# Optimization experiments

Hardware: AMD Instinct MI355X
Metric: run time of the kernel (lower is better)

## Reference

```python
import jax, jax.numpy as jnp
import numpy as np

BN_EPS = 1e-5


def setup_inputs() -> dict:
    key = jax.random.key(0)
    ks = jax.random.split(key, 6)
    N, E, D_IN, D_OUT = 100000, 625000, 128, 128
    x = jax.random.normal(ks[0], (N, D_IN), dtype=jnp.float32)
    edge_index = jax.random.randint(ks[1], (2, E), 0, N, dtype=jnp.int64)
    # Glorot-style init for GCNConv weight, uniform for linear (values only matter for correctness testing)
    W = jax.random.normal(ks[2], (D_IN, D_OUT), dtype=jnp.float32) * (1.0 / np.sqrt(D_IN))
    b = jnp.zeros((D_OUT,), dtype=jnp.float32)
    res_W = jax.random.normal(ks[3], (D_IN, D_OUT), dtype=jnp.float32) * (1.0 / np.sqrt(D_IN))
    res_b = jnp.zeros((D_OUT,), dtype=jnp.float32)
    bn_gamma = jnp.ones((D_OUT,), dtype=jnp.float32)
    bn_beta = jnp.zeros((D_OUT,), dtype=jnp.float32)
    return {"x": x, "edge_index": edge_index, "W": W, "b": b,
            "res_W": res_W, "res_b": res_b, "bn_gamma": bn_gamma, "bn_beta": bn_beta}


def _gcn_forward(x, edge_index, W, b, res_W, res_b, bn_gamma, bn_beta):
    N = x.shape[0]
    # ---- GCNConv: add self-loops, symmetric degree normalization (PyG defaults) ----
    loops = jnp.arange(N, dtype=edge_index.dtype)
    src = jnp.concatenate([edge_index[0], loops])  # row (source)
    dst = jnp.concatenate([edge_index[1], loops])  # col (target)
    ones = jnp.ones(src.shape[0], dtype=x.dtype)
    deg = jax.ops.segment_sum(ones, dst, num_segments=N)  # in-degree incl. self-loop
    deg_inv_sqrt = jnp.where(deg > 0, jax.lax.rsqrt(deg), 0.0)
    norm = deg_inv_sqrt[src] * deg_inv_sqrt[dst]  # [E+N]
    # transform first (dense GEMM), then gather/scale/scatter-add
    h = x @ W  # [N, D_OUT]
    msg = h[src] * norm[:, None]  # gather + scale
    agg = jax.ops.segment_sum(msg, dst, num_segments=N) + b  # scatter-add + bias
    # ---- residual: relu(linear(x)) ----
    res = jax.nn.relu(x @ res_W + res_b)
    y = agg + res
    # ---- dropout(p=0.0) is identity; BatchNorm1d (training mode, batch stats) ----
    mean = jnp.mean(y, axis=0)
    var = jnp.mean(jnp.square(y - mean), axis=0)  # biased variance, as in torch BN normalization
    y = (y - mean) * jax.lax.rsqrt(var + BN_EPS) * bn_gamma + bn_beta
    return y


def reference(x, edge_index, W, b, res_W, res_b, bn_gamma, bn_beta):
    return _gcn_forward(x, edge_index, W, b, res_W, res_b, bn_gamma, bn_beta)
```

## Files before the change

kernel.cpp:

```cpp
#include <hip/hip_runtime.h>
#include <math.h>

#define D 128
#define DW 64

typedef __attribute__((ext_vector_type(8))) short bf16x8;
typedef __attribute__((ext_vector_type(4))) float f32x4;
union U4 { uint4 u; bf16x8 f; };

__device__ __forceinline__ float blo(unsigned p){ return __uint_as_float(p << 16); }
__device__ __forceinline__ float bhi(unsigned p){ return __uint_as_float(p & 0xffff0000u); }
__device__ __forceinline__ unsigned bpack(float a, float b){
  unsigned x = __float_as_uint(a), y = __float_as_uint(b);
  x += 0x7fffu + ((x >> 16) & 1u);
  y += 0x7fffu + ((y >> 16) & 1u);
  return (x >> 16) | (y & 0xffff0000u);
}


__global__ void k_deg(const int* __restrict__ ei, int* __restrict__ cnt, int E){
  int e = blockIdx.x*256 + threadIdx.x;
  if (e < E) atomicAdd(cnt + ei[E + e], 1);
}

__global__ void k_scan1(const int* __restrict__ cnt, int* __restrict__ off,
                        int* __restrict__ bsum, int N){
  __shared__ int sm[256];
  int i = blockIdx.x*256 + threadIdx.x;
  int v = (i < N) ? cnt[i] : 0;
  int acc = v;
  sm[threadIdx.x] = acc;
  __syncthreads();
  for (int s = 1; s < 256; s <<= 1){
    int t = (threadIdx.x >= s) ? sm[threadIdx.x - s] : 0;
    __syncthreads();
    acc += t;
    sm[threadIdx.x] = acc;
    __syncthreads();
  }
  if (i < N) off[i] = acc - v;
  if (threadIdx.x == 255) bsum[blockIdx.x] = acc;
}

__global__ void k_scan2(int* __restrict__ bsum, int nb){
  __shared__ int sm[512];
  int v = (threadIdx.x < nb) ? bsum[threadIdx.x] : 0;
  int acc = v;
  sm[threadIdx.x] = acc;
  __syncthreads();
  for (int s = 1; s < 512; s <<= 1){
    int t = (threadIdx.x >= s) ? sm[threadIdx.x - s] : 0;
    __syncthreads();
    acc += t;
    sm[threadIdx.x] = acc;
    __syncthreads();
  }
  if (threadIdx.x < nb) bsum[threadIdx.x] = acc - v;
}

__global__ void k_scan3(int* __restrict__ off, const int* __restrict__ bsum,
                        int* __restrict__ cursor, int N){
  int i = blockIdx.x*256 + threadIdx.x;
  if (i < N){
    int o = off[i] + bsum[blockIdx.x];
    off[i] = o;
    cursor[i] = o;
  }
}

__global__ void k_prep(const float* __restrict__ x, const int* __restrict__ cnt,
                       unsigned* __restrict__ out_u, int N){
  int idx = blockIdx.x*256 + threadIdx.x;
  if (idx >= N*32) return;
  int row = idx >> 5, q = idx & 31;
  float dis = rsqrtf((float)(cnt[row] + 1));
  float4 xv = reinterpret_cast<const float4*>(x)[idx];
  uint2 r; r.x = bpack(xv.x*dis, xv.y*dis); r.y = bpack(xv.z*dis, xv.w*dis);
  reinterpret_cast<uint2*>(out_u)[(size_t)row*64 + 32 + q] = r;
}

__global__ void k_wprep(const float* __restrict__ W, const float* __restrict__ RW,
                        unsigned* __restrict__ dst){
  int idx = blockIdx.x*256 + threadIdx.x;
  int m = idx >> 13;
  int w = idx & 8191;
  int c = w >> 6, kd = w & 63;
  const float* src = m ? RW : W;
  float a = src[(2*kd)*128 + c];
  float b = src[(2*kd+1)*128 + c];
  dst[(m<<13) + c*64 + (kd ^ ((c & 7) << 2))] = bpack(a, b);
}

__global__ void k_fill(const int* __restrict__ ei, int* __restrict__ cursor,
                       int* __restrict__ elist, int E){
  int e = blockIdx.x*256 + threadIdx.x;
  if (e < E){
    int d = ei[E + e];
    int pos = atomicAdd(cursor + d, 1);
    elist[pos] = ei[e];
  }
}

__global__ __launch_bounds__(256) void k_agg(unsigned* __restrict__ out_u,
    const int* __restrict__ elist, const int* __restrict__ off,
    const int* __restrict__ cnt, int N){
  const int lane = threadIdx.x & 63;
  int wid = blockIdx.x*4 + (threadIdx.x >> 6);
  const int nw = gridDim.x*4;
  for (int i = wid; i < N; i += nw){
    int node = __builtin_amdgcn_readfirstlane(i);
    int o = off[node];
    int c = cnt[node];
    unsigned ps = out_u[(size_t)node*128 + 64 + lane];
    float a0 = 0.f, a1 = 0.f;
    for (int j0 = 0; j0 < c; j0 += 64){
      int m = c - j0; if (m > 64) m = 64;
      int li = lane < m ? lane : m-1;
      int sid = elist[o + j0 + li];
      for (int jj = 0; jj < m; jj += 4){
        int s0 = __shfl(sid, jj);
        int s1 = __shfl(sid, jj+1 < m ? jj+1 : m-1);
        int s2 = __shfl(sid, jj+2 < m ? jj+2 : m-1);
        int s3 = __shfl(sid, jj+3 < m ? jj+3 : m-1);
        unsigned p0 = out_u[(size_t)s0*128 + 64 + lane];
        unsigned p1 = out_u[(size_t)s1*128 + 64 + lane];
        unsigned p2 = out_u[(size_t)s2*128 + 64 + lane];
        unsigned p3 = out_u[(size_t)s3*128 + 64 + lane];
        if (jj+1 >= m) p1 = 0;
        if (jj+2 >= m) p2 = 0;
        if (jj+3 >= m) p3 = 0;
        a0 += blo(p0) + blo(p1) + blo(p2) + blo(p3);
        a1 += bhi(p0) + bhi(p1) + bhi(p2) + bhi(p3);
      }
    }
    a0 += blo(ps); a1 += bhi(ps);
    float dis = rsqrtf((float)(c + 1));
    out_u[(size_t)node*128 + lane] = bpack(a0*dis, a1*dis);
  }
}

__global__ __launch_bounds__(512) void k_gemm(
    const unsigned* __restrict__ wsW,
    const float* __restrict__ bias, const float* __restrict__ rbias,
    const int* __restrict__ cnt,
    float* __restrict__ out, float* __restrict__ colsum, int N)
{
  __shared__ unsigned lds[16384];
  unsigned* out_u = reinterpret_cast<unsigned*>(out);
  for (int i = threadIdx.x; i < 16384; i += 512) lds[i] = wsW[i];
  __syncthreads();

  const int lane = threadIdx.x & 63;
  const int wave = threadIdx.x >> 6;
  const int lo = lane & 15, hi = lane >> 4;
  const int rowbase = (blockIdx.x * 8 + wave) * 16;

  float bcol[8], rbcol[8];
  #pragma unroll
  for (int ct = 0; ct < 8; ++ct){
    bcol[ct]  = bias[ct*16 + lo];
    rbcol[ct] = rbias[ct*16 + lo];
  }

  int arow = rowbase + lo; if (arow >= N) arow = N - 1;
  U4 aggF[4], xbF[4];
  #pragma unroll
  for (int kk = 0; kk < 4; ++kk){
    aggF[kk].u = *(const uint4*)&out_u[(size_t)arow*128 + kk*16 + hi*4];
    xbF[kk].u  = *(const uint4*)&out_u[(size_t)arow*128 + 64 + kk*16 + hi*4];
  }

  f32x4 accA[8], accR[8];
  #pragma unroll
  for (int ct = 0; ct < 8; ++ct){
    accA[ct] = (f32x4){0.f,0.f,0.f,0.f};
    accR[ct] = (f32x4){0.f,0.f,0.f,0.f};
  }

  #pragma unroll
  for (int ct = 0; ct < 8; ++ct){
    const int c = ct*16 + lo;
    #pragma unroll
    for (int kk = 0; kk < 4; ++kk){
      int kd = (kk*16 + hi*4) ^ ((c & 7) << 2);
      U4 wf, rf;
      wf.u = *(const uint4*)&lds[c*64 + kd];
      rf.u = *(const uint4*)&lds[8192 + c*64 + kd];
      accA[ct] = __builtin_amdgcn_mfma_f32_16x16x32_bf16(aggF[kk].f, wf.f, accA[ct], 0,0,0);
      accR[ct] = __builtin_amdgcn_mfma_f32_16x16x32_bf16(xbF[kk].f, rf.f, accR[ct], 0,0,0);
    }
  }

  float s_[4];
  #pragma unroll
  for (int j = 0; j < 4; ++j){
    int r = rowbase + hi*4 + j;
    int rc = r < N ? r : N - 1;
    s_[j] = sqrtf((float)(cnt[rc] + 1));
  }
  float cs[8], cq[8];
  #pragma unroll
  for (int ct = 0; ct < 8; ++ct){ cs[ct] = 0.f; cq[ct] = 0.f; }

  #pragma unroll
  for (int ct = 0; ct < 8; ++ct){
    const int col = ct*16 + lo;
    #pragma unroll
    for (int j = 0; j < 4; ++j){
      int r = rowbase + hi*4 + j;
      if (r < N){
        float y = accA[ct][j] + bcol[ct] + fmaxf(accR[ct][j]*s_[j] + rbcol[ct], 0.f);
        out[(size_t)r*128 + col] = y;
        cs[ct] += y; cq[ct] += y*y;
      }
    }
  }

  #pragma unroll
  for (int ct = 0; ct < 8; ++ct){
    cs[ct] += __shfl_xor(cs[ct], 16); cs[ct] += __shfl_xor(cs[ct], 32);
    cq[ct] += __shfl_xor(cq[ct], 16); cq[ct] += __shfl_xor(cq[ct], 32);
  }
  __syncthreads();
  float* red = reinterpret_cast<float*>(lds);
  if (lane < 16){
    #pragma unroll
    for (int ct = 0; ct < 8; ++ct){
      int col = ct*16 + lane;
      red[wave*256 + 2*col]     = cs[ct];
      red[wave*256 + 2*col + 1] = cq[ct];
    }
  }
  __syncthreads();
  if (threadIdx.x < 256){
    float t = 0.f;
    #pragma unroll
    for (int w = 0; w < 8; ++w) t += red[w*256 + threadIdx.x];
    atomicAdd(colsum + threadIdx.x, t);
  }
}

__global__ void k_norm(float4* __restrict__ out4, const float* __restrict__ colsum,
                       const float* __restrict__ gamma, const float* __restrict__ beta,
                       float fN, int n4){
  __shared__ float sc[256];
  if (threadIdx.x < 128){
    int c = threadIdx.x;
    float mean = colsum[2*c] / fN;
    float var  = fmaxf(colsum[2*c + 1] / fN - mean*mean, 0.f);
    float s = gamma[c] * rsqrtf(var + 1e-5f);
    sc[c] = s;
    sc[128 + c] = beta[c] - mean * s;
  }
  __syncthreads();
  const float4* s4 = reinterpret_cast<const float4*>(sc);
  int idx = blockIdx.x*256 + threadIdx.x;
  int stride = gridDim.x*256;
  for (int i = idx; i < n4; i += stride){
    int cb = i & 31;
    float4 v = out4[i];
    float4 s = s4[cb];
    float4 t = s4[32 + cb];
    v.x = v.x*s.x + t.x; v.y = v.y*s.y + t.y;
    v.z = v.z*s.z + t.z; v.w = v.w*s.w + t.w;
    out4[i] = v;
  }
}

extern "C" void kernel_launch(void* const* d_in, const int* in_sizes, int n_in,
                              void* d_out, int out_size, void* d_ws, size_t ws_size,
                              hipStream_t stream){
  const float* x     = (const float*)d_in[0];
  const int*   ei    = (const int*)d_in[1];
  const float* W     = (const float*)d_in[2];
  const float* b     = (const float*)d_in[3];
  const float* RW    = (const float*)d_in[4];
  const float* rb    = (const float*)d_in[5];
  const float* gamma = (const float*)d_in[6];
  const float* beta  = (const float*)d_in[7];
  float* out = (float*)d_out;
  unsigned* out_u = (unsigned*)d_out;
  const int N = in_sizes[0] / D;
  const int E = in_sizes[1] / 2;

  char* ws = (char*)d_ws;
  size_t o = 0;
  auto alloc = [&](size_t bytes)->void*{
    void* p = ws + o;
    o += (bytes + 255) & ~size_t(255);
    return p;
  };
  int*      cnt    = (int*)alloc((size_t)N*4);
  int*      off    = (int*)alloc((size_t)N*4);
  int*      cursor = (int*)alloc((size_t)N*4);
  int*      bsum   = (int*)alloc(512*4);
  float*    colsum = (float*)alloc(256*4);
  unsigned* wsW    = (unsigned*)alloc(16384*4);
  int*      elist  = (int*)alloc((size_t)E*4);

  hipMemsetAsync(cnt, 0, (size_t)N*4, stream);
  hipMemsetAsync(colsum, 0, 256*4, stream);

  int egrid = (E + 255)/256;
  int nb = (N + 255)/256;
  k_deg  <<<egrid, 256, 0, stream>>>(ei, cnt, E);
  k_scan1<<<nb,    256, 0, stream>>>(cnt, off, bsum, N);
  k_scan2<<<1,     512, 0, stream>>>(bsum, nb);
  k_scan3<<<nb,    256, 0, stream>>>(off, bsum, cursor, N);
  k_prep <<<(N*32 + 255)/256, 256, 0, stream>>>(x, cnt, out_u, N);
  k_wprep<<<64,    256, 0, stream>>>(W, RW, wsW);
  k_fill <<<egrid, 256, 0, stream>>>(ei, cursor, elist, E);
  k_agg  <<<4096,  256, 0, stream>>>(out_u, elist, off, cnt, N);
  k_gemm <<<(N + 127)/128, 512, 0, stream>>>(wsW, b, rb, cnt, out, colsum, N);
  k_norm <<<2048,  256, 0, stream>>>((float4*)out, colsum, gamma, beta, (float)N, N*32);
}
```

Baseline: 269.9 us.

## Fuse GEMM and BatchNorm into one persistent kernel with grid barrier

Merges the GEMM/residual kernel and the normalization kernel into one persistent launch of 512 blocks, each handling two 128-row tiles. The pre-norm outputs are kept in registers as packed bf16 and finished with a software grid-wide atomic barrier after the column statistics are reduced. This removes the separate pass that wrote fp32 outputs and then read and rewrote them. In exchange it requires all 512 blocks to be co-resident (launch_bounds 512,4 with 64KB LDS each) or the barrier deadlocks. It also adds bf16 rounding of y before normalization.

```diff
diff --git a/kernel.cpp b/kernel.cpp
--- a/kernel.cpp
+++ b/kernel.cpp
@@ -2,7 +2,6 @@
 #include <math.h>
 
 #define D 128
-#define DW 64
 
 typedef __attribute__((ext_vector_type(8))) short bf16x8;
 typedef __attribute__((ext_vector_type(4))) float f32x4;
@@ -139,29 +138,13 @@
   }
 }
 
-__global__ __launch_bounds__(512) void k_gemm(
-    const unsigned* __restrict__ wsW,
+__device__ __forceinline__ void gemm_tile(int rowbase, int N,
+    const unsigned* __restrict__ out_u, const unsigned* lds,
+    int lo, int hi,
     const float* __restrict__ bias, const float* __restrict__ rbias,
     const int* __restrict__ cnt,
-    float* __restrict__ out, float* __restrict__ colsum, int N)
+    unsigned* __restrict__ yp, float* __restrict__ cs, float* __restrict__ cq)
 {
-  __shared__ unsigned lds[16384];
-  unsigned* out_u = reinterpret_cast<unsigned*>(out);
-  for (int i = threadIdx.x; i < 16384; i += 512) lds[i] = wsW[i];
-  __syncthreads();
-
-  const int lane = threadIdx.x & 63;
-  const int wave = threadIdx.x >> 6;
-  const int lo = lane & 15, hi = lane >> 4;
-  const int rowbase = (blockIdx.x * 8 + wave) * 16;
-
-  float bcol[8], rbcol[8];
-  #pragma unroll
-  for (int ct = 0; ct < 8; ++ct){
-    bcol[ct]  = bias[ct*16 + lo];
-    rbcol[ct] = rbias[ct*16 + lo];
-  }
-
   int arow = rowbase + lo; if (arow >= N) arow = N - 1;
   U4 aggF[4], xbF[4];
   #pragma unroll
@@ -169,14 +152,12 @@
     aggF[kk].u = *(const uint4*)&out_u[(size_t)arow*128 + kk*16 + hi*4];
     xbF[kk].u  = *(const uint4*)&out_u[(size_t)arow*128 + 64 + kk*16 + hi*4];
   }
-
   f32x4 accA[8], accR[8];
   #pragma unroll
   for (int ct = 0; ct < 8; ++ct){
     accA[ct] = (f32x4){0.f,0.f,0.f,0.f};
     accR[ct] = (f32x4){0.f,0.f,0.f,0.f};
   }
-
   #pragma unroll
   for (int ct = 0; ct < 8; ++ct){
     const int c = ct*16 + lo;
@@ -190,7 +171,6 @@
       accR[ct] = __builtin_amdgcn_mfma_f32_16x16x32_bf16(xbF[kk].f, rf.f, accR[ct], 0,0,0);
     }
   }
-
   float s_[4];
   #pragma unroll
   for (int j = 0; j < 4; ++j){
@@ -198,23 +178,71 @@
     int rc = r < N ? r : N - 1;
     s_[j] = sqrtf((float)(cnt[rc] + 1));
   }
-  float cs[8], cq[8];
-  #pragma unroll
-  for (int ct = 0; ct < 8; ++ct){ cs[ct] = 0.f; cq[ct] = 0.f; }
-
-  #pragma unroll
-  for (int ct = 0; ct < 8; ++ct){
-    const int col = ct*16 + lo;
-    #pragma unroll
-    for (int j = 0; j < 4; ++j){
-      int r = rowbase + hi*4 + j;
-      if (r < N){
-        float y = accA[ct][j] + bcol[ct] + fmaxf(accR[ct][j]*s_[j] + rbcol[ct], 0.f);
-        out[(size_t)r*128 + col] = y;
-        cs[ct] += y; cq[ct] += y*y;
-      }
-    }
-  }
+  const int rb = rowbase + hi*4;
+  #pragma unroll
+  for (int ct = 0; ct < 8; ++ct){
+    float bc  = bias[ct*16 + lo];
+    float rbc = rbias[ct*16 + lo];
+    float y0 = accA[ct][0] + bc + fmaxf(accR[ct][0]*s_[0] + rbc, 0.f);
+    float y1 = accA[ct][1] + bc + fmaxf(accR[ct][1]*s_[1] + rbc, 0.f);
+    float y2 = accA[ct][2] + bc + fmaxf(accR[ct][2]*s_[2] + rbc, 0.f);
+    float y3 = accA[ct][3] + bc + fmaxf(accR[ct][3]*s_[3] + rbc, 0.f);
+    if (rb + 0 < N){ cs[ct] += y0; cq[ct] += y0*y0; }
+    if (rb + 1 < N){ cs[ct] += y1; cq[ct] += y1*y1; }
+    if (rb + 2 < N){ cs[ct] += y2; cq[ct] += y2*y2; }
+    if (rb + 3 < N){ cs[ct] += y3; cq[ct] += y3*y3; }
+    yp[2*ct]   = bpack(y0, y1);
+    yp[2*ct+1] = bpack(y2, y3);
+  }
+}
+
+__device__ __forceinline__ void norm_tile(int rowbase, int N, float* __restrict__ out,
+    int lo, int hi, const float* sc, const unsigned* __restrict__ yp)
+{
+  const int rb = rowbase + hi*4;
+  #pragma unroll
+  for (int ct = 0; ct < 8; ++ct){
+    int col = ct*16 + lo;
+    float s = sc[col], t = sc[128 + col];
+    float y0 = blo(yp[2*ct]),   y1 = bhi(yp[2*ct]);
+    float y2 = blo(yp[2*ct+1]), y3 = bhi(yp[2*ct+1]);
+    if (rb + 0 < N) out[(size_t)(rb+0)*128 + col] = y0*s + t;
+    if (rb + 1 < N) out[(size_t)(rb+1)*128 + col] = y1*s + t;
+    if (rb + 2 < N) out[(size_t)(rb+2)*128 + col] = y2*s + t;
+    if (rb + 3 < N) out[(size_t)(rb+3)*128 + col] = y3*s + t;
+  }
+}
+
+__global__ __launch_bounds__(512, 4) void k_gemm_norm(
+    const unsigned* __restrict__ wsW,
+    const float* __restrict__ bias, const float* __restrict__ rbias,
+    const int* __restrict__ cnt,
+    float* __restrict__ out, float* __restrict__ colsum,
+    unsigned* __restrict__ bar,
+    const float* __restrict__ gamma, const float* __restrict__ beta,
+    int N, int nt, float fN)
+{
+  __shared__ unsigned lds[16384];
+  unsigned* out_u = reinterpret_cast<unsigned*>(out);
+  for (int i = threadIdx.x; i < 16384; i += 512) lds[i] = wsW[i];
+  __syncthreads();
+
+  const int lane = threadIdx.x & 63;
+  const int wave = threadIdx.x >> 6;
+  const int lo = lane & 15, hi = lane >> 4;
+
+  int t0 = blockIdx.x;
+  int t1 = blockIdx.x + gridDim.x;
+  bool has0 = (t0 < nt);
+  bool has1 = (t1 < nt);
+  int rb0 = t0*128 + wave*16;
+  int rb1 = t1*128 + wave*16;
+
+  unsigned yp0[16], yp1[16];
+  float cs[8] = {0,0,0,0,0,0,0,0}, cq[8] = {0,0,0,0,0,0,0,0};
+
+  if (has0) gemm_tile(rb0, N, out_u, lds, lo, hi, bias, rbias, cnt, yp0, cs, cq);
+  if (has1) gemm_tile(rb1, N, out_u, lds, lo, hi, bias, rbias, cnt, yp1, cs, cq);
 
   #pragma unroll
   for (int ct = 0; ct < 8; ++ct){
@@ -238,33 +266,31 @@
     for (int w = 0; w < 8; ++w) t += red[w*256 + threadIdx.x];
     atomicAdd(colsum + threadIdx.x, t);
   }
-}
-
-__global__ void k_norm(float4* __restrict__ out4, const float* __restrict__ colsum,
-                       const float* __restrict__ gamma, const float* __restrict__ beta,
-                       float fN, int n4){
-  __shared__ float sc[256];
+
+  __syncthreads();
+  if (threadIdx.x == 0){
+    __threadfence();
+    __hip_atomic_fetch_add(bar, 1u, __ATOMIC_ACQ_REL, __HIP_MEMORY_SCOPE_AGENT);
+    while (__hip_atomic_load(bar, __ATOMIC_ACQUIRE, __HIP_MEMORY_SCOPE_AGENT)
+           < (unsigned)gridDim.x) {}
+  }
+  __syncthreads();
+
+  float* sc = reinterpret_cast<float*>(lds);
   if (threadIdx.x < 128){
     int c = threadIdx.x;
-    float mean = colsum[2*c] / fN;
-    float var  = fmaxf(colsum[2*c + 1] / fN - mean*mean, 0.f);
+    float s0 = __hip_atomic_load(&colsum[2*c],     __ATOMIC_RELAXED, __HIP_MEMORY_SCOPE_AGENT);
+    float s1 = __hip_atomic_load(&colsum[2*c + 1], __ATOMIC_RELAXED, __HIP_MEMORY_SCOPE_AGENT);
+    float mean = s0 / fN;
+    float var  = fmaxf(s1 / fN - mean*mean, 0.f);
     float s = gamma[c] * rsqrtf(var + 1e-5f);
     sc[c] = s;
     sc[128 + c] = beta[c] - mean * s;
   }
   __syncthreads();
-  const float4* s4 = reinterpret_cast<const float4*>(sc);
-  int idx = blockIdx.x*256 + threadIdx.x;
-  int stride = gridDim.x*256;
-  for (int i = idx; i < n4; i += stride){
-    int cb = i & 31;
-    float4 v = out4[i];
-    float4 s = s4[cb];
-    float4 t = s4[32 + cb];
-    v.x = v.x*s.x + t.x; v.y = v.y*s.y + t.y;
-    v.z = v.z*s.z + t.z; v.w = v.w*s.w + t.w;
-    out4[i] = v;
-  }
+
+  if (has0) norm_tile(rb0, N, out, lo, hi, sc, yp0);
+  if (has1) norm_tile(rb1, N, out, lo, hi, sc, yp1);
 }
 
 extern "C" void kernel_launch(void* const* d_in, const int* in_sizes, int n_in,
@@ -295,14 +321,16 @@
   int*      cursor = (int*)alloc((size_t)N*4);
   int*      bsum   = (int*)alloc(512*4);
   float*    colsum = (float*)alloc(256*4);
+  unsigned* bar    = (unsigned*)alloc(256);
   unsigned* wsW    = (unsigned*)alloc(16384*4);
   int*      elist  = (int*)alloc((size_t)E*4);
 
   hipMemsetAsync(cnt, 0, (size_t)N*4, stream);
-  hipMemsetAsync(colsum, 0, 256*4, stream);
+  hipMemsetAsync(colsum, 0, 256*4 + 256, stream);
 
   int egrid = (E + 255)/256;
   int nb = (N + 255)/256;
+  int nt = (N + 127)/128;
   k_deg  <<<egrid, 256, 0, stream>>>(ei, cnt, E);
   k_scan1<<<nb,    256, 0, stream>>>(cnt, off, bsum, N);
   k_scan2<<<1,     512, 0, stream>>>(bsum, nb);
@@ -311,6 +339,6 @@
   k_wprep<<<64,    256, 0, stream>>>(W, RW, wsW);
   k_fill <<<egrid, 256, 0, stream>>>(ei, cursor, elist, E);
   k_agg  <<<4096,  256, 0, stream>>>(out_u, elist, off, cnt, N);
-  k_gemm <<<(N + 127)/128, 512, 0, stream>>>(wsW, b, rb, cnt, out, colsum, N);
-  k_norm <<<2048,  256, 0, stream>>>((float4*)out, colsum, gamma, beta, (float)N, N*32);
-}
+  k_gemm_norm<<<512, 512, 0, stream>>>(wsW, b, rb, cnt, out, colsum, bar,
+                                       gamma, beta, N, nt, (float)N);
+}
```

After: 308.7 us. +14.4%, slower.
